# Kernel tuning notes

Measured on AMD Instinct MI355X. Metric: run time of the kernel, lower is better.

## Reference

```python
import jax, jax.numpy as jnp
import numpy as np

K = 3          # B-spline order (cubic)
G = 10         # number of spline intervals over [0, 1]
NELY, NELX = 512, 512
WIDTHS = [2, 32, 32, 1]


def _make_grid(in_dim):
    # extended uniform knot vector over [0,1] with K extra knots each side: (in_dim, G+2K+1)
    h = 1.0 / G
    knots = jnp.arange(-K, G + K + 1, dtype=jnp.float32) * h
    return jnp.tile(knots[None, :], (in_dim, 1))


def setup_inputs() -> dict:
    key = jax.random.key(0)
    ks = jax.random.split(key, 1 + 3 * (len(WIDTHS) - 1))
    inp = {"coords": jax.random.uniform(ks[0], (NELY * NELX, 2), dtype=jnp.float32)}
    for l, (i, o) in enumerate(zip(WIDTHS[:-1], WIDTHS[1:])):
        inp[f"grid{l}"] = _make_grid(i)
        inp[f"coef{l}"] = 0.1 * jax.random.normal(ks[1 + 3 * l], (i, o, G + K), dtype=jnp.float32)
        inp[f"sb{l}"] = jax.random.normal(ks[2 + 3 * l], (i, o), dtype=jnp.float32) / np.sqrt(i).astype(np.float32)
        inp[f"sp{l}"] = jnp.ones((i, o), dtype=jnp.float32)
    inp["density_bias"] = jnp.full((1,), np.float32(np.log(0.5 / (1.0 - 0.5 + 1e-8))))
    return inp


def _b_batch(x, grid):
    # Cox-de Boor recursion. x: (B, in), grid: (in, G+2K+1) -> bases (B, in, G+K)
    xe = x[:, :, None]
    v = ((xe >= grid[None, :, :-1]) & (xe < grid[None, :, 1:])).astype(x.dtype)
    for p in range(1, K + 1):
        left = (xe - grid[None, :, : -(p + 1)]) / (grid[None, :, p:-1] - grid[None, :, : -(p + 1)])
        right = (grid[None, :, p + 1:] - xe) / (grid[None, :, p + 1:] - grid[None, :, 1:-p])
        v = left * v[:, :, :-1] + right * v[:, :, 1:]
    return v


def _kan_layer(x, grid, coef, sb, sp):
    # y_out = sum_in [ sb * silu(x) + sp * sum_k B_k(x) * coef_k ]
    B = _b_batch(x, grid)                               # (batch, in, G+K)
    spline = jnp.einsum('bik,iok->bio', B, coef)        # (batch, in, out)
    base = jax.nn.silu(x)                               # (batch, in)
    return jnp.sum(sb[None] * base[:, :, None] + sp[None] * spline, axis=1)


def reference(coords, grid0, coef0, sb0, sp0, grid1, coef1, sb1, sp1,
              grid2, coef2, sb2, sp2, density_bias):
    h = _kan_layer(coords, grid0, coef0, sb0, sp0)
    h = _kan_layer(h, grid1, coef1, sb1, sp1)
    logits = _kan_layer(h, grid2, coef2, sb2, sp2) + density_bias
    return jax.nn.sigmoid(logits).reshape(1, NELY, NELX)
```

## Files before the change

kernel.cpp:

```cpp
#include <hip/hip_runtime.h>
#include <hip/hip_bf16.h>

typedef __hip_bfloat16 bf16;
typedef __fp16 h2v __attribute__((ext_vector_type(2)));
typedef __fp16 half8 __attribute__((ext_vector_type(8)));
typedef float floatx4 __attribute__((ext_vector_type(4)));

#define NPTS (512*512)

#define OFF_BIAS 12
#define OFF_FLAG 13
#define OFF_BF   16
#define NFRAG    34
#define OFF_LIN  (16 + NFRAG*256)
#define LIN_WORDS 640


__device__ __forceinline__ bool sniff_f32(const void* g0) {
    float f = ((const float*)g0)[0];
    return fabsf(f + 0.3f) < 0.01f;
}
__device__ __forceinline__ float ld(const void* p, int i, bool f32) {
    return f32 ? ((const float*)p)[i] : __bfloat162float(((const bf16*)p)[i]);
}
__device__ __forceinline__ unsigned pk_rtn(float a, float b) {
    union { h2v v; unsigned u; } x;
    x.v[0] = (__fp16)a; x.v[1] = (__fp16)b;
    return x.u;
}
__device__ __forceinline__ unsigned pkf16(float a, float b) {
    union { h2v v; unsigned u; } x;
    x.v = __builtin_amdgcn_cvt_pkrtz(a, b);
    return x.u;
}

__device__ float slotval(int layer, int K, int o,
                         const void* c0, const void* sb0, const void* sp0,
                         const void* c1, const void* sb1, const void* sp1,
                         bool f32)
{
    int i = K >> 4, s = K & 15;
    if (s >= 1 && s <= 13) {
        int m = s - 1;
        if (layer == 0) return ld(c0, (i*32+o)*13 + m, f32) * ld(sp0, i*32+o, f32);
        return ld(c1, (i*32+o)*13 + m, f32) * ld(sp1, i*32+o, f32);
    }
    if (s == 14) {
        if (layer == 0) return ld(sb0, i*32+o, f32);
        return ld(sb1, i*32+o, f32);
    }
    return 0.0f;
}

__global__ __launch_bounds__(256) void kan_prep(
    const void* __restrict__ g0, const void* __restrict__ c0,
    const void* __restrict__ sb0, const void* __restrict__ sp0,
    const void* __restrict__ g1, const void* __restrict__ c1,
    const void* __restrict__ sb1, const void* __restrict__ sp1,
    const void* __restrict__ g2, const void* __restrict__ c2,
    const void* __restrict__ sb2, const void* __restrict__ sp2,
    const void* __restrict__ bias, float* __restrict__ ws)
{
    const bool f32 = sniff_f32(g0);
    int t = blockIdx.x * blockDim.x + threadIdx.x;

    if (t < 16) {
        if (t < 12) {
            int l = t >> 2, j = t & 3;
            const void* g = (l == 0) ? g0 : (l == 1) ? g1 : g2;
            float lo = ld(g, 0, f32), hi = ld(g, 16, f32);
            float ih = 16.0f / (hi - lo);
            float v = (j == 0) ? lo : (j == 1) ? hi
                    : (j == 2) ? ih : (-lo * ih);
            ws[t] = v;
        } else if (t == 12) ws[12] = ld(bias, 0, f32);
        else if (t == 13)   ws[13] = f32 ? 1.0f : 0.0f;
        else                ws[t] = 0.0f;
        return;
    }
    int ft = t - 16;
    if (ft < NFRAG * 64) {
        int f = ft >> 6, l = ft & 63, n = l & 15, q = l >> 4;
        int layer, c, nt;
        if (f < 2) { layer = 0; c = 0;            nt = f; }
        else       { layer = 1; c = (f - 2) >> 1; nt = (f - 2) & 1; }
        int o = nt * 16 + n;
        unsigned wv[4];
#pragma unroll
        for (int jp = 0; jp < 4; jp++) {
            int K0 = c * 32 + q * 8 + jp * 2;
            float v0 = slotval(layer, K0,     o, c0,sb0,sp0, c1,sb1,sp1, f32);
            float v1 = slotval(layer, K0 + 1, o, c0,sb0,sp0, c1,sb1,sp1, f32);
            wv[jp] = pk_rtn(v0, v1);
        }
        uint4 out4; out4.x = wv[0]; out4.y = wv[1]; out4.z = wv[2]; out4.w = wv[3];
        ((uint4*)((unsigned*)ws + OFF_BF))[f * 64 + l] = out4;
        return;
    }
    int w2 = ft - NFRAG * 64;
    if (w2 < LIN_WORDS) {
        int i = w2 / 20, j = w2 - i * 20;
        float v = 0.0f;
        if (j >= 3 && j <= 15) v = ld(c2, i*13 + (j - 3), f32) * ld(sp2, i, f32);
        else if (j == 19)      v = ld(sb2, i, f32);
        ws[OFF_LIN + w2] = v;
    }
}

__device__ __forceinline__ floatx4 mf(uint4 a, uint4 b, floatx4 c)
{
    union { uint4 u; half8 h; } ua, ub;
    ua.u = a; ub.u = b;
    return __builtin_amdgcn_mfma_f32_16x16x32_f16(ua.h, ub.h, c, 0, 0, 0);
}

__device__ __forceinline__ void eval_taps(float x, float ngh, float ih,
    unsigned& A, unsigned& B, unsigned& C, int& wout, float& si)
{
    float t  = fmaf(x, ih, ngh);
    float fj = floorf(t);
    float u  = t - fj;
    bool inb = (t >= 0.0f) && (t < 16.0f);
    float s6 = inb ? 0.166666667f : 0.0f;
    int jc = min(max((int)fj, 0), 15);
    float u2 = u * u, u3 = u2 * u, om = 1.0f - u;
    float b0 = om * om * om * s6;
    float b1 = (fmaf(3.0f, u3, 4.0f) - 6.0f * u2) * s6;
    float b2 = fmaf(-3.0f, u3, fmaf(3.0f, u2, fmaf(3.0f, u, 1.0f))) * s6;
    float b3 = u3 * s6;
    int s0 = jc - 2;
    wout = ((s0 + 2) >> 1) - 1;
    if (s0 & 1) { A = pkf16(0.0f, b0); B = pkf16(b1, b2); C = pkf16(b3, 0.0f); }
    else        { A = pkf16(b0, b1);   B = pkf16(b2, b3); C = 0u; }
    si = x / (1.0f + __expf(-x));
}

struct TapPack {
    unsigned A0, B0, C0, A1, B1, C1, S0, S1;
    int w0, w1;
};

__device__ __forceinline__ TapPack eval2(float f0, float f1,
                                         float ngh, float ih)
{
    TapPack t;
    float si0, si1;
    eval_taps(f0, ngh, ih, t.A0, t.B0, t.C0, t.w0, si0);
    eval_taps(f1, ngh, ih, t.A1, t.B1, t.C1, t.w1, si1);
    t.S0 = pkf16(si0, 0.0f);
    t.S1 = pkf16(si1, 0.0f);
    return t;
}

__device__ __forceinline__ void commit(unsigned* row, const TapPack& t)
{
    uint4 z; z.x = 0u; z.y = 0u; z.z = 0u; z.w = 0u;
    *(uint4*)(row + 0)  = z;
    *(uint4*)(row + 4)  = z;
    *(uint4*)(row + 8)  = z;
    *(uint4*)(row + 12) = z;
    row[t.w0 < 0 ? 18 : t.w0] = t.A0;
    row[t.w0 + 1]  = t.B0;
    row[t.w0 + 2]  = t.C0;
    row[8 + t.w1]  = t.A1;
    row[9 + t.w1]  = t.B1;
    row[10 + t.w1] = t.C1;
    row[7]  = t.S0;
    row[15] = t.S1;
}

__global__ __launch_bounds__(256, 4) void kan_main(
    const void* __restrict__ coords, const float* __restrict__ ws,
    void* __restrict__ out)
{
    __shared__ __align__(16) unsigned lds[4 * 1280 + LIN_WORDS];
    const unsigned* wsu = (const unsigned*)ws;
    const uint4* bfp = (const uint4*)(wsu + OFF_BF);

    int tid = threadIdx.x;
    int l = tid & 63, w = tid >> 6;
    int p = blockIdx.x * 256 + w * 64 + l;

    unsigned* lin2s = lds + 4 * 1280;
#pragma unroll
    for (int j = 0; j < 3; j++) {
        int idx = tid + j * 256;
        if (idx < LIN_WORDS) lin2s[idx] = wsu[OFF_LIN + idx];
    }
    __syncthreads();

    unsigned* rb = lds + w * 1280;
    unsigned* cb = rb;
    unsigned* myrow = cb + l * 20;

    const bool f32 = (ws[OFF_FLAG] != 0.0f);
    float x0, x1;
    if (f32) {
        float2 c = ((const float2*)coords)[p];
        x0 = c.x; x1 = c.y;
    } else {
        unsigned cc = ((const unsigned*)coords)[p];
        union { unsigned u; float f; } cv;
        cv.u = (cc & 0xffffu) << 16;  x0 = cv.f;
        cv.u = cc & 0xffff0000u;      x1 = cv.f;
    }

    const float iha = ws[2],  ngha = ws[3];
    const float ihb = ws[6],  nghb = ws[7];
    const float ihc = ws[10], nghc = ws[11];

    const int arow = l & 15, aq = (l >> 4) * 4;
    const int drow = (l >> 4) * 4, dcol = l & 15;

    float h[32];

    {
        floatx4 acc[4][2];
#pragma unroll
        for (int mt = 0; mt < 4; mt++)
#pragma unroll
            for (int nt = 0; nt < 2; nt++) acc[mt][nt] = (floatx4)0.0f;

        uint4 bf0 = bfp[0 * 64 + l], bf1 = bfp[1 * 64 + l];
        TapPack t0 = eval2(x0, x1, ngha, iha);
        commit(myrow, t0);
#pragma unroll
        for (int mt = 0; mt < 4; mt++) {
            uint4 a = *(const uint4*)(cb + (arow + 16 * mt) * 20 + aq);
            acc[mt][0] = mf(a, bf0, acc[mt][0]);
            acc[mt][1] = mf(a, bf1, acc[mt][1]);
        }
#pragma unroll
        for (int nt = 0; nt < 2; nt++) {
#pragma unroll
            for (int mt = 0; mt < 4; mt++)
#pragma unroll
                for (int r = 0; r < 4; r++)
                    rb[(mt*16 + drow + r) * 20 + dcol] =
                        __float_as_uint(acc[mt][nt][r]);
#pragma unroll
            for (int q = 0; q < 4; q++) {
                uint4 v = *(const uint4*)(rb + l * 20 + q * 4);
                h[nt*16 + q*4+0] = __uint_as_float(v.x);
                h[nt*16 + q*4+1] = __uint_as_float(v.y);
                h[nt*16 + q*4+2] = __uint_as_float(v.z);
                h[nt*16 + q*4+3] = __uint_as_float(v.w);
            }
        }
    }

    {
        floatx4 acc[4][2];
#pragma unroll
        for (int mt = 0; mt < 4; mt++)
#pragma unroll
            for (int nt = 0; nt < 2; nt++) acc[mt][nt] = (floatx4)0.0f;

        uint4 bf0 = bfp[2 * 64 + l], bf1 = bfp[3 * 64 + l];
        {
            TapPack t0 = eval2(h[0], h[1], nghb, ihb);
            commit(myrow, t0);
        }
#pragma unroll
        for (int c = 0; c < 16; c++) {
            uint4 nbf0, nbf1; TapPack tn;
            if (c < 15) {
                nbf0 = bfp[(4 + 2*c) * 64 + l];
                nbf1 = bfp[(5 + 2*c) * 64 + l];
                tn = eval2(h[2*c + 2], h[2*c + 3], nghb, ihb);
            }
#pragma unroll
            for (int mt = 0; mt < 4; mt++) {
                uint4 a = *(const uint4*)(cb + (arow + 16 * mt) * 20 + aq);
                acc[mt][0] = mf(a, bf0, acc[mt][0]);
                acc[mt][1] = mf(a, bf1, acc[mt][1]);
            }
            if (c < 15) { commit(myrow, tn); bf0 = nbf0; bf1 = nbf1; }
        }
#pragma unroll
        for (int nt = 0; nt < 2; nt++) {
#pragma unroll
            for (int mt = 0; mt < 4; mt++)
#pragma unroll
                for (int r = 0; r < 4; r++)
                    rb[(mt*16 + drow + r) * 20 + dcol] =
                        __float_as_uint(acc[mt][nt][r]);
#pragma unroll
            for (int q = 0; q < 4; q++) {
                uint4 v = *(const uint4*)(rb + l * 20 + q * 4);
                h[nt*16 + q*4+0] = __uint_as_float(v.x);
                h[nt*16 + q*4+1] = __uint_as_float(v.y);
                h[nt*16 + q*4+2] = __uint_as_float(v.z);
                h[nt*16 + q*4+3] = __uint_as_float(v.w);
            }
        }
    }

    {
        const float* l2t = (const float*)lin2s;
        float z0 = ws[OFF_BIAS], z1 = 0.0f, z2 = 0.0f, z3 = 0.0f;
#pragma unroll
        for (int i = 0; i < 32; i++) {
            float x = h[i];
            float t  = fmaf(x, ihc, nghc);
            float fj = floorf(t);
            float u  = t - fj;
            bool inb = (t >= 0.0f) && (t < 16.0f);
            float s6 = inb ? 0.166666667f : 0.0f;
            int jc = min(max((int)fj, 0), 15);
            float u2 = u * u, u3 = u2 * u, om = 1.0f - u;
            float b0 = om * om * om * s6;
            float b1 = (fmaf(3.0f, u3, 4.0f) - 6.0f * u2) * s6;
            float b2 = fmaf(-3.0f, u3, fmaf(3.0f, u2, fmaf(3.0f, u, 1.0f))) * s6;
            float b3 = u3 * s6;
            const float* row = l2t + i * 20;
            float si = x / (1.0f + __expf(-x));
            z0 = fmaf(b0, row[jc + 0], z0);
            z1 = fmaf(b1, row[jc + 1], z1);
            z2 = fmaf(b2, row[jc + 2], z2);
            z3 = fmaf(b3, row[jc + 3], z3);
            z0 = fmaf(si, row[19], z0);
        }
        float z = (z0 + z1) + (z2 + z3);
        float r = 1.0f / (1.0f + __expf(-z));
        if (f32) ((float*)out)[p] = r;
        else     ((bf16*)out)[p] = __float2bfloat16(r);
    }
}

extern "C" void kernel_launch(void* const* d_in, const int* in_sizes, int n_in,
                              void* d_out, int out_size, void* d_ws, size_t ws_size,
                              hipStream_t stream)
{
    float* ws = (float*)d_ws;

    kan_prep<<<(16 + NFRAG*64 + LIN_WORDS + 255) / 256, 256, 0, stream>>>(
        d_in[1], d_in[2], d_in[3], d_in[4],
        d_in[5], d_in[6], d_in[7], d_in[8],
        d_in[9], d_in[10], d_in[11], d_in[12],
        d_in[13], ws);

    kan_main<<<NPTS / 256, 256, 0, stream>>>(d_in[0], ws, d_out);
}
```

Baseline: 112.2 us.

## Split each point across two lanes to halve per-thread spline work

Each wavefront now handles 32 points instead of 64. The two half-waves each evaluate the spline taps for one of the paired inputs and each own half of the final-layer sum, which is combined with a cross-lane shuffle. This halves the per-thread serial basis evaluation and the MFMA M-tiles per wave, and shrinks LDS per block. The price is twice as many blocks, duplicated weight-fragment loads per point, and half the lanes idle at the store. The software prefetch of the next fragment and taps in the layer-2 loop is also removed.

```diff
diff --git a/kernel.cpp b/kernel.cpp
--- a/kernel.cpp
+++ b/kernel.cpp
@@ -135,53 +135,42 @@
     si = x / (1.0f + __expf(-x));
 }
 
-struct TapPack {
-    unsigned A0, B0, C0, A1, B1, C1, S0, S1;
-    int w0, w1;
-};
-
-__device__ __forceinline__ TapPack eval2(float f0, float f1,
-                                         float ngh, float ih)
-{
-    TapPack t;
-    float si0, si1;
-    eval_taps(f0, ngh, ih, t.A0, t.B0, t.C0, t.w0, si0);
-    eval_taps(f1, ngh, ih, t.A1, t.B1, t.C1, t.w1, si1);
-    t.S0 = pkf16(si0, 0.0f);
-    t.S1 = pkf16(si1, 0.0f);
+struct Tap1 { unsigned A, B, C, S; int w; };
+
+__device__ __forceinline__ Tap1 eval1(float x, float ngh, float ih)
+{
+    Tap1 t; float si;
+    eval_taps(x, ngh, ih, t.A, t.B, t.C, t.w, si);
+    t.S = pkf16(si, 0.0f);
     return t;
 }
 
-__device__ __forceinline__ void commit(unsigned* row, const TapPack& t)
+__device__ __forceinline__ void commit32(unsigned* row, int hb, const Tap1& t)
 {
     uint4 z; z.x = 0u; z.y = 0u; z.z = 0u; z.w = 0u;
-    *(uint4*)(row + 0)  = z;
-    *(uint4*)(row + 4)  = z;
-    *(uint4*)(row + 8)  = z;
-    *(uint4*)(row + 12) = z;
-    row[t.w0 < 0 ? 18 : t.w0] = t.A0;
-    row[t.w0 + 1]  = t.B0;
-    row[t.w0 + 2]  = t.C0;
-    row[8 + t.w1]  = t.A1;
-    row[9 + t.w1]  = t.B1;
-    row[10 + t.w1] = t.C1;
-    row[7]  = t.S0;
-    row[15] = t.S1;
+    *(uint4*)(row + hb)     = z;
+    *(uint4*)(row + hb + 4) = z;
+    int base = hb + t.w;
+    row[base + 2] = t.C;
+    row[base + 1] = t.B;
+    row[base < 0 ? 18 : base] = t.A;
+    row[hb + 7] = t.S;
 }
 
 __global__ __launch_bounds__(256, 4) void kan_main(
     const void* __restrict__ coords, const float* __restrict__ ws,
     void* __restrict__ out)
 {
-    __shared__ __align__(16) unsigned lds[4 * 1280 + LIN_WORDS];
+    __shared__ __align__(16) unsigned lds[4 * 640 + LIN_WORDS];
     const unsigned* wsu = (const unsigned*)ws;
     const uint4* bfp = (const uint4*)(wsu + OFF_BF);
 
     int tid = threadIdx.x;
     int l = tid & 63, w = tid >> 6;
-    int p = blockIdx.x * 256 + w * 64 + l;
-
-    unsigned* lin2s = lds + 4 * 1280;
+    int pt = l & 31, hf = l >> 5;
+    int p = blockIdx.x * 128 + w * 32 + pt;
+
+    unsigned* lin2s = lds + 4 * 640;
 #pragma unroll
     for (int j = 0; j < 3; j++) {
         int idx = tid + j * 256;
@@ -189,9 +178,10 @@
     }
     __syncthreads();
 
-    unsigned* rb = lds + w * 1280;
+    unsigned* rb = lds + w * 640;
     unsigned* cb = rb;
-    unsigned* myrow = cb + l * 20;
+    unsigned* myrow = cb + pt * 20;
+    const int hb = hf * 8;
 
     const bool f32 = (ws[OFF_FLAG] != 0.0f);
     float x0, x1;
@@ -215,17 +205,17 @@
     float h[32];
 
     {
-        floatx4 acc[4][2];
-#pragma unroll
-        for (int mt = 0; mt < 4; mt++)
+        floatx4 acc[2][2];
+#pragma unroll
+        for (int mt = 0; mt < 2; mt++)
 #pragma unroll
             for (int nt = 0; nt < 2; nt++) acc[mt][nt] = (floatx4)0.0f;
 
         uint4 bf0 = bfp[0 * 64 + l], bf1 = bfp[1 * 64 + l];
-        TapPack t0 = eval2(x0, x1, ngha, iha);
-        commit(myrow, t0);
-#pragma unroll
-        for (int mt = 0; mt < 4; mt++) {
+        Tap1 t0 = eval1(hf ? x1 : x0, ngha, iha);
+        commit32(myrow, hb, t0);
+#pragma unroll
+        for (int mt = 0; mt < 2; mt++) {
             uint4 a = *(const uint4*)(cb + (arow + 16 * mt) * 20 + aq);
             acc[mt][0] = mf(a, bf0, acc[mt][0]);
             acc[mt][1] = mf(a, bf1, acc[mt][1]);
@@ -233,14 +223,14 @@
 #pragma unroll
         for (int nt = 0; nt < 2; nt++) {
 #pragma unroll
-            for (int mt = 0; mt < 4; mt++)
+            for (int mt = 0; mt < 2; mt++)
 #pragma unroll
                 for (int r = 0; r < 4; r++)
                     rb[(mt*16 + drow + r) * 20 + dcol] =
                         __float_as_uint(acc[mt][nt][r]);
 #pragma unroll
             for (int q = 0; q < 4; q++) {
-                uint4 v = *(const uint4*)(rb + l * 20 + q * 4);
+                uint4 v = *(const uint4*)(rb + pt * 20 + q * 4);
                 h[nt*16 + q*4+0] = __uint_as_float(v.x);
                 h[nt*16 + q*4+1] = __uint_as_float(v.y);
                 h[nt*16 + q*4+2] = __uint_as_float(v.z);
@@ -250,44 +240,37 @@
     }
 
     {
-        floatx4 acc[4][2];
-#pragma unroll
-        for (int mt = 0; mt < 4; mt++)
+        floatx4 acc[2][2];
+#pragma unroll
+        for (int mt = 0; mt < 2; mt++)
 #pragma unroll
             for (int nt = 0; nt < 2; nt++) acc[mt][nt] = (floatx4)0.0f;
 
-        uint4 bf0 = bfp[2 * 64 + l], bf1 = bfp[3 * 64 + l];
-        {
-            TapPack t0 = eval2(h[0], h[1], nghb, ihb);
-            commit(myrow, t0);
-        }
 #pragma unroll
         for (int c = 0; c < 16; c++) {
-            uint4 nbf0, nbf1; TapPack tn;
-            if (c < 15) {
-                nbf0 = bfp[(4 + 2*c) * 64 + l];
-                nbf1 = bfp[(5 + 2*c) * 64 + l];
-                tn = eval2(h[2*c + 2], h[2*c + 3], nghb, ihb);
-            }
-#pragma unroll
-            for (int mt = 0; mt < 4; mt++) {
+            uint4 bf0 = bfp[(2 + 2*c) * 64 + l];
+            uint4 bf1 = bfp[(3 + 2*c) * 64 + l];
+            float xf = hf ? h[2*c + 1] : h[2*c];
+            Tap1 tn = eval1(xf, nghb, ihb);
+            commit32(myrow, hb, tn);
+#pragma unroll
+            for (int mt = 0; mt < 2; mt++) {
                 uint4 a = *(const uint4*)(cb + (arow + 16 * mt) * 20 + aq);
                 acc[mt][0] = mf(a, bf0, acc[mt][0]);
                 acc[mt][1] = mf(a, bf1, acc[mt][1]);
             }
-            if (c < 15) { commit(myrow, tn); bf0 = nbf0; bf1 = nbf1; }
         }
 #pragma unroll
         for (int nt = 0; nt < 2; nt++) {
 #pragma unroll
-            for (int mt = 0; mt < 4; mt++)
+            for (int mt = 0; mt < 2; mt++)
 #pragma unroll
                 for (int r = 0; r < 4; r++)
                     rb[(mt*16 + drow + r) * 20 + dcol] =
                         __float_as_uint(acc[mt][nt][r]);
 #pragma unroll
             for (int q = 0; q < 4; q++) {
-                uint4 v = *(const uint4*)(rb + l * 20 + q * 4);
+                uint4 v = *(const uint4*)(rb + pt * 20 + q * 4);
                 h[nt*16 + q*4+0] = __uint_as_float(v.x);
                 h[nt*16 + q*4+1] = __uint_as_float(v.y);
                 h[nt*16 + q*4+2] = __uint_as_float(v.z);
@@ -297,11 +280,11 @@
     }
 
     {
-        const float* l2t = (const float*)lin2s;
-        float z0 = ws[OFF_BIAS], z1 = 0.0f, z2 = 0.0f, z3 = 0.0f;
-#pragma unroll
-        for (int i = 0; i < 32; i++) {
-            float x = h[i];
+        const float* l2t = (const float*)lin2s + hf * 320;
+        float z0 = 0.0f, z1 = 0.0f, z2 = 0.0f, z3 = 0.0f;
+#pragma unroll
+        for (int i = 0; i < 16; i++) {
+            float x = hf ? h[16 + i] : h[i];
             float t  = fmaf(x, ihc, nghc);
             float fj = floorf(t);
             float u  = t - fj;
@@ -322,9 +305,13 @@
             z0 = fmaf(si, row[19], z0);
         }
         float z = (z0 + z1) + (z2 + z3);
+        z += __shfl_xor(z, 32);
+        z += ws[OFF_BIAS];
         float r = 1.0f / (1.0f + __expf(-z));
-        if (f32) ((float*)out)[p] = r;
-        else     ((bf16*)out)[p] = __float2bfloat16(r);
+        if (hf == 0) {
+            if (f32) ((float*)out)[p] = r;
+            else     ((bf16*)out)[p] = __float2bfloat16(r);
+        }
     }
 }
 
@@ -340,5 +327,5 @@
         d_in[9], d_in[10], d_in[11], d_in[12],
         d_in[13], ws);
 
-    kan_main<<<NPTS / 256, 256, 0, stream>>>(d_in[0], ws, d_out);
-}
+    kan_main<<<NPTS / 128, 256, 0, stream>>>(d_in[0], ws, d_out);
+}
```

Result: faster. 109.8 us (-2.1%).
